# Kernel tuning notes

Hardware: AMD Instinct MI355X
Metric: run time of the kernel (lower is better)

Reference implementation:

```python
import jax, jax.numpy as jnp
import numpy as np

N_USERS = 50000
N_ITEMS = 10000
N_ENTITIES = 40000
N_NODES = N_USERS + N_ITEMS + N_ENTITIES  # 100000
EMB = 64
NNZ = 1600000  # avg degree 16
VIS_DIM = 2048
TXT_DIM = 300


def setup_inputs() -> dict:
    key = jax.random.key(0)
    ks = jax.random.split(key, 16)
    def xn(k, shape, scale=0.05):
        return jax.random.normal(k, shape, dtype=jnp.float32) * scale
    return {
        "adj_row": jax.random.randint(ks[0], (NNZ,), 0, N_NODES, dtype=jnp.int32),
        "adj_col": jax.random.randint(ks[1], (NNZ,), 0, N_NODES, dtype=jnp.int32),
        "adj_val": jax.random.uniform(ks[2], (NNZ,), dtype=jnp.float32) / 16.0,  # ~normalized adj
        "embedding": xn(ks[3], (N_NODES, EMB), 0.1),
        "visual_features": jax.random.normal(ks[4], (N_ITEMS, VIS_DIM), dtype=jnp.float32),
        "text_features": jax.random.normal(ks[5], (N_ITEMS, TXT_DIM), dtype=jnp.float32),
        "Wv1": xn(ks[6], (512, VIS_DIM)), "bv1": jnp.zeros((512,), jnp.float32),
        "Wv2": xn(ks[7], (EMB, 512)),    "bv2": jnp.zeros((EMB,), jnp.float32),
        "Wt1": xn(ks[8], (256, TXT_DIM)), "bt1": jnp.zeros((256,), jnp.float32),
        "Wt2": xn(ks[9], (EMB, 256)),    "bt2": jnp.zeros((EMB,), jnp.float32),
        "Wd": xn(ks[10], (EMB, EMB)),    "bd": jnp.zeros((EMB,), jnp.float32),
        "Wc0": xn(ks[11], (EMB, 2 * EMB)), "bc0": jnp.zeros((EMB,), jnp.float32),
        "Wc1": xn(ks[12], (EMB, 2 * EMB)), "bc1": jnp.zeros((EMB,), jnp.float32),
    }


def _lin(x, W, b):
    return x @ W.T + b


def reference(adj_row, adj_col, adj_val, embedding, visual_features, text_features,
              Wv1, bv1, Wv2, bv2, Wt1, bt1, Wt2, bt2, Wd, bd, Wc0, bc0, Wc1, bc1):
    # multimodal item encoding (eval mode: dropout = identity)
    vis = _lin(jax.nn.relu(_lin(visual_features, Wv1, bv1)), Wv2, bv2)
    vis = _lin(vis, Wd, bd)
    txt = _lin(jax.nn.relu(_lin(text_features, Wt1, bt1)), Wt2, bt2)
    txt = _lin(txt, Wd, bd)
    fused_item = (vis + txt) * 0.5  # [n_items, emb]

    ego = embedding.at[N_USERS:N_USERS + N_ITEMS].set(fused_item)

    all_embs = [ego]
    cur = ego
    for Wc, bc in ((Wc0, bc0), (Wc1, bc1)):
        # SpMM: neighbor[i] = sum_j A[i,j] * cur[j]
        msgs = adj_val[:, None] * cur[adj_col]            # [nnz, emb]
        nb = jax.ops.segment_sum(msgs, adj_row, num_segments=N_NODES)
        cur = _lin(jnp.concatenate([cur, nb], axis=-1), Wc, bc)  # W_concat
        cur = jax.nn.leaky_relu(cur, 0.01)                # F.leaky_relu default slope
        all_embs.append(cur)

    return jnp.concatenate(all_embs, axis=-1)  # [n_nodes, emb*(n_layers+1)]
```

## Files before the change

kernel.cpp:

```cpp
#include <hip/hip_runtime.h>
#include <hip/hip_bf16.h>
#include <cstddef>

#define N_USERS 50000
#define N_ITEMS 10000
#define N_NODES 100000
#define EMB 64
#define NNZ_E 1600000
#define VIS_DIM 2048
#define TXT_DIM 300

typedef short bf16x8 __attribute__((ext_vector_type(8)));
typedef float f32x4  __attribute__((ext_vector_type(4)));

__device__ inline unsigned short f2bf(float x) {
    __hip_bfloat16 h = __float2bfloat16(x);
    return __builtin_bit_cast(unsigned short, h);
}
__device__ inline float bf2f(unsigned short u) {
    unsigned int t = ((unsigned int)u) << 16;
    float f;
    __builtin_memcpy(&f, &t, 4);
    return f;
}

template<int MI, int NI>
__global__ __launch_bounds__(256) void gemm_dg(
    const float* __restrict__ A, const float* __restrict__ W,
    const float* __restrict__ bias, float* __restrict__ C,
    int M, int N, int K, int k_per, long long c_plane,
    int act, int add_bias)
{
    const int t   = threadIdx.x;
    const int w   = t >> 6;
    const int l   = t & 63;
    const int l16 = l & 15;
    const int lq  = l >> 4;

    const int n0 = blockIdx.x * (NI * 16);
    const int m0 = (blockIdx.y * 4 + w) * (MI * 16);
    if (m0 >= M) return;
    const int kz = blockIdx.z;
    const int kb = kz * k_per;
    int krem = K - kb; if (krem > k_per) krem = k_per;
    const int kiters = (krem + 31) / 32;
    float* Cz = C + (long long)kz * c_plane;

    const float* ap[MI];
    #pragma unroll
    for (int mi = 0; mi < MI; mi++) {
        int r = m0 + mi * 16 + l16; if (r >= M) r = M - 1;
        ap[mi] = A + (size_t)r * K;
    }
    const float* wpt[NI];
    #pragma unroll
    for (int ni = 0; ni < NI; ni++) {
        int r = n0 + ni * 16 + l16; if (r >= N) r = N - 1;
        wpt[ni] = W + (size_t)r * K;
    }

    f32x4 acc[MI][NI] = {};

    for (int kt = 0; kt < kiters; kt++) {
        const int k0 = kb + kt * 32 + lq * 8;

        bf16x8 ahi[MI], alo[MI];
        #pragma unroll
        for (int mi = 0; mi < MI; mi++) {
            float v[8];
            if (k0 + 7 < K) {
                float4 q0 = *(const float4*)(ap[mi] + k0);
                float4 q1 = *(const float4*)(ap[mi] + k0 + 4);
                v[0]=q0.x; v[1]=q0.y; v[2]=q0.z; v[3]=q0.w;
                v[4]=q1.x; v[5]=q1.y; v[6]=q1.z; v[7]=q1.w;
            } else {
                #pragma unroll
                for (int i = 0; i < 8; i++)
                    v[i] = (k0 + i < K) ? ap[mi][k0 + i] : 0.f;
            }
            #pragma unroll
            for (int i = 0; i < 8; i++) {
                unsigned short h = f2bf(v[i]);
                ahi[mi][i] = (short)h;
                alo[mi][i] = (short)f2bf(v[i] - bf2f(h));
            }
        }

        bf16x8 whi[NI], wlo[NI];
        #pragma unroll
        for (int ni = 0; ni < NI; ni++) {
            float v[8];
            if (k0 + 7 < K) {
                float4 q0 = *(const float4*)(wpt[ni] + k0);
                float4 q1 = *(const float4*)(wpt[ni] + k0 + 4);
                v[0]=q0.x; v[1]=q0.y; v[2]=q0.z; v[3]=q0.w;
                v[4]=q1.x; v[5]=q1.y; v[6]=q1.z; v[7]=q1.w;
            } else {
                #pragma unroll
                for (int i = 0; i < 8; i++)
                    v[i] = (k0 + i < K) ? wpt[ni][k0 + i] : 0.f;
            }
            #pragma unroll
            for (int i = 0; i < 8; i++) {
                unsigned short h = f2bf(v[i]);
                whi[ni][i] = (short)h;
                wlo[ni][i] = (short)f2bf(v[i] - bf2f(h));
            }
        }

        #pragma unroll
        for (int ni = 0; ni < NI; ni++) {
            #pragma unroll
            for (int mi = 0; mi < MI; mi++) {
                acc[mi][ni] = __builtin_amdgcn_mfma_f32_16x16x32_bf16(
                    ahi[mi], whi[ni], acc[mi][ni], 0, 0, 0);
                acc[mi][ni] = __builtin_amdgcn_mfma_f32_16x16x32_bf16(
                    ahi[mi], wlo[ni], acc[mi][ni], 0, 0, 0);
                acc[mi][ni] = __builtin_amdgcn_mfma_f32_16x16x32_bf16(
                    alo[mi], whi[ni], acc[mi][ni], 0, 0, 0);
            }
        }
    }

    #pragma unroll
    for (int ni = 0; ni < NI; ni++) {
        int col = n0 + ni * 16 + l16;
        if (col >= N) continue;
        float b = (add_bias && kz == 0) ? bias[col] : 0.f;
        #pragma unroll
        for (int mi = 0; mi < MI; mi++) {
            #pragma unroll
            for (int r = 0; r < 4; r++) {
                int row = m0 + mi * 16 + lq * 4 + r;
                if (row >= M) continue;
                float vv = acc[mi][ni][r] + b;
                if (act) vv = fmaxf(vv, 0.f);
                Cz[(size_t)row * N + col] = vv;
            }
        }
    }
}

#define GLDW 40

__global__ __launch_bounds__(256, 2) void concat_mfma(
    const float* __restrict__ cur, const float* __restrict__ nbuf,
    const float* __restrict__ Wc, const float* __restrict__ bias,
    float* __restrict__ out_cur, float* __restrict__ out_full, int col_off)
{
    __shared__ unsigned short Ah[128][GLDW], Al[128][GLDW];
    __shared__ unsigned short Bh[64][GLDW],  Bl[64][GLDW];

    const int t   = threadIdx.x;
    const int w   = t >> 6;
    const int l   = t & 63;
    const int l16 = l & 15;
    const int lq  = l >> 4;
    const int m0  = blockIdx.x * 128;
    const int mh  = w * 32;

    const int r  = t >> 2;
    const int kc = t & 3;

    f32x4 acc[2][4] = {};

    float pa[2][8], pw[8];

    auto load_tile = [&](int kt) {
        const float* src = (kt < 2) ? cur : nbuf;
        const int kcol = (kt & 1) * 32 + kc * 8;
        #pragma unroll
        for (int p = 0; p < 2; p++) {
            int rg = m0 + r + p * 64;
            if (rg >= N_NODES) rg = N_NODES - 1;
            const float* g = src + (size_t)rg * 64 + kcol;
            float4 q0 = *(const float4*)g, q1 = *(const float4*)(g + 4);
            pa[p][0]=q0.x; pa[p][1]=q0.y; pa[p][2]=q0.z; pa[p][3]=q0.w;
            pa[p][4]=q1.x; pa[p][5]=q1.y; pa[p][6]=q1.z; pa[p][7]=q1.w;
        }
        const float* gw = Wc + (size_t)r * 128 + kt * 32 + kc * 8;
        float4 q0 = *(const float4*)gw, q1 = *(const float4*)(gw + 4);
        pw[0]=q0.x; pw[1]=q0.y; pw[2]=q0.z; pw[3]=q0.w;
        pw[4]=q1.x; pw[5]=q1.y; pw[6]=q1.z; pw[7]=q1.w;
    };

    load_tile(0);

    for (int kt = 0; kt < 4; kt++) {
        #pragma unroll
        for (int p = 0; p < 2; p++) {
            bf16x8 hi, lo;
            #pragma unroll
            for (int i = 0; i < 8; i++) {
                unsigned short h = f2bf(pa[p][i]);
                hi[i] = (short)h;
                lo[i] = (short)f2bf(pa[p][i] - bf2f(h));
            }
            *(bf16x8*)&Ah[r + p * 64][kc * 8] = hi;
            *(bf16x8*)&Al[r + p * 64][kc * 8] = lo;
        }
        {
            bf16x8 hi, lo;
            #pragma unroll
            for (int i = 0; i < 8; i++) {
                unsigned short h = f2bf(pw[i]);
                hi[i] = (short)h;
                lo[i] = (short)f2bf(pw[i] - bf2f(h));
            }
            *(bf16x8*)&Bh[r][kc * 8] = hi;
            *(bf16x8*)&Bl[r][kc * 8] = lo;
        }
        __syncthreads();

        if (kt < 3) load_tile(kt + 1);

        {
            bf16x8 ah[2], al[2];
            #pragma unroll
            for (int mi = 0; mi < 2; mi++) {
                ah[mi] = *(const bf16x8*)&Ah[mh + mi * 16 + l16][lq * 8];
                al[mi] = *(const bf16x8*)&Al[mh + mi * 16 + l16][lq * 8];
            }
            #pragma unroll
            for (int ni = 0; ni < 4; ni++) {
                bf16x8 bh = *(const bf16x8*)&Bh[ni * 16 + l16][lq * 8];
                bf16x8 bl = *(const bf16x8*)&Bl[ni * 16 + l16][lq * 8];
                #pragma unroll
                for (int mi = 0; mi < 2; mi++) {
                    acc[mi][ni] = __builtin_amdgcn_mfma_f32_16x16x32_bf16(
                        ah[mi], bh, acc[mi][ni], 0, 0, 0);
                    acc[mi][ni] = __builtin_amdgcn_mfma_f32_16x16x32_bf16(
                        ah[mi], bl, acc[mi][ni], 0, 0, 0);
                    acc[mi][ni] = __builtin_amdgcn_mfma_f32_16x16x32_bf16(
                        al[mi], bh, acc[mi][ni], 0, 0, 0);
                }
            }
        }
        __syncthreads();
    }

    #pragma unroll
    for (int ni = 0; ni < 4; ni++) {
        int col = ni * 16 + l16;
        float bcol = bias[col];
        #pragma unroll
        for (int mi = 0; mi < 2; mi++) {
            #pragma unroll
            for (int rr = 0; rr < 4; rr++) {
                int row = m0 + mh + mi * 16 + lq * 4 + rr;
                if (row >= N_NODES) continue;
                float v = acc[mi][ni][rr] + bcol;
                v = (v > 0.f) ? v : 0.01f * v;
                if (out_cur) out_cur[(size_t)row * 64 + col] = v;
                out_full[(size_t)row * 192 + col_off + col] = v;
            }
        }
    }
}

__global__ void transp64(const float* __restrict__ W, float* __restrict__ wT, int K)
{
    int i = blockIdx.x * 256 + threadIdx.x;
    if (i >= 64 * K) return;
    int d = i / K, k = i - d * K;
    wT[k * 64 + d] = W[i];
}

__global__ __launch_bounds__(256) void linear64(
    const float* __restrict__ in, const float* __restrict__ in2,
    const float* __restrict__ wT, const float* __restrict__ bias,
    float* __restrict__ out, int M, int K, float in_scale, int add,
    int fuse_relu)
{
    int t  = threadIdx.x;
    int d  = t & 63;
    int w  = t >> 6;
    int m0 = blockIdx.x * 16 + w * 4;
    if (m0 >= M) return;
    int mlast = M - 1;
    int m1 = (m0 + 1 < M) ? m0 + 1 : mlast;
    int m2 = (m0 + 2 < M) ? m0 + 2 : mlast;
    int m3 = (m0 + 3 < M) ? m0 + 3 : mlast;

    const float* x0 = in + (size_t)m0 * K;
    const float* x1 = in + (size_t)m1 * K;
    const float* x2 = in + (size_t)m2 * K;
    const float* x3 = in + (size_t)m3 * K;
    const float* y0 = fuse_relu ? in2 + (size_t)m0 * K : x0;
    const float* y1 = fuse_relu ? in2 + (size_t)m1 * K : x1;
    const float* y2 = fuse_relu ? in2 + (size_t)m2 * K : x2;
    const float* y3 = fuse_relu ? in2 + (size_t)m3 * K : x3;

    float a0 = 0.f, a1 = 0.f, a2 = 0.f, a3 = 0.f;

    for (int k = 0; k < K; k += 8) {
        const float* wp = wT + (size_t)k * 64 + d;
        float w0 = wp[0],   w1 = wp[64],  w2 = wp[128], w3 = wp[192];
        float w4 = wp[256], w5 = wp[320], w6 = wp[384], w7 = wp[448];
        float4 p0 = *(const float4*)(x0 + k), q0 = *(const float4*)(x0 + k + 4);
        float4 p1 = *(const float4*)(x1 + k), q1 = *(const float4*)(x1 + k + 4);
        float4 p2 = *(const float4*)(x2 + k), q2 = *(const float4*)(x2 + k + 4);
        float4 p3 = *(const float4*)(x3 + k), q3 = *(const float4*)(x3 + k + 4);
        if (fuse_relu) {
            float4 r0 = *(const float4*)(y0 + k), s0 = *(const float4*)(y0 + k + 4);
            float4 r1 = *(const float4*)(y1 + k), s1 = *(const float4*)(y1 + k + 4);
            float4 r2 = *(const float4*)(y2 + k), s2 = *(const float4*)(y2 + k + 4);
            float4 r3 = *(const float4*)(y3 + k), s3 = *(const float4*)(y3 + k + 4);
            p0.x=fmaxf(p0.x+r0.x,0.f); p0.y=fmaxf(p0.y+r0.y,0.f);
            p0.z=fmaxf(p0.z+r0.z,0.f); p0.w=fmaxf(p0.w+r0.w,0.f);
            q0.x=fmaxf(q0.x+s0.x,0.f); q0.y=fmaxf(q0.y+s0.y,0.f);
            q0.z=fmaxf(q0.z+s0.z,0.f); q0.w=fmaxf(q0.w+s0.w,0.f);
            p1.x=fmaxf(p1.x+r1.x,0.f); p1.y=fmaxf(p1.y+r1.y,0.f);
            p1.z=fmaxf(p1.z+r1.z,0.f); p1.w=fmaxf(p1.w+r1.w,0.f);
            q1.x=fmaxf(q1.x+s1.x,0.f); q1.y=fmaxf(q1.y+s1.y,0.f);
            q1.z=fmaxf(q1.z+s1.z,0.f); q1.w=fmaxf(q1.w+s1.w,0.f);
            p2.x=fmaxf(p2.x+r2.x,0.f); p2.y=fmaxf(p2.y+r2.y,0.f);
            p2.z=fmaxf(p2.z+r2.z,0.f); p2.w=fmaxf(p2.w+r2.w,0.f);
            q2.x=fmaxf(q2.x+s2.x,0.f); q2.y=fmaxf(q2.y+s2.y,0.f);
            q2.z=fmaxf(q2.z+s2.z,0.f); q2.w=fmaxf(q2.w+s2.w,0.f);
            p3.x=fmaxf(p3.x+r3.x,0.f); p3.y=fmaxf(p3.y+r3.y,0.f);
            p3.z=fmaxf(p3.z+r3.z,0.f); p3.w=fmaxf(p3.w+r3.w,0.f);
            q3.x=fmaxf(q3.x+s3.x,0.f); q3.y=fmaxf(q3.y+s3.y,0.f);
            q3.z=fmaxf(q3.z+s3.z,0.f); q3.w=fmaxf(q3.w+s3.w,0.f);
        }
        a0 += p0.x*w0 + p0.y*w1 + p0.z*w2 + p0.w*w3
            + q0.x*w4 + q0.y*w5 + q0.z*w6 + q0.w*w7;
        a1 += p1.x*w0 + p1.y*w1 + p1.z*w2 + p1.w*w3
            + q1.x*w4 + q1.y*w5 + q1.z*w6 + q1.w*w7;
        a2 += p2.x*w0 + p2.y*w1 + p2.z*w2 + p2.w*w3
            + q2.x*w4 + q2.y*w5 + q2.z*w6 + q2.w*w7;
        a3 += p3.x*w0 + p3.y*w1 + p3.z*w2 + p3.w*w3
            + q3.x*w4 + q3.y*w5 + q3.z*w6 + q3.w*w7;
    }

    float b = bias[d];
    float r0 = a0 * in_scale + b;
    float r1 = a1 * in_scale + b;
    float r2 = a2 * in_scale + b;
    float r3 = a3 * in_scale + b;
    if (add) {
        out[(size_t)m0 * 64 + d] += r0;
        if (m0 + 1 < M) out[(size_t)m1 * 64 + d] += r1;
        if (m0 + 2 < M) out[(size_t)m2 * 64 + d] += r2;
        if (m0 + 3 < M) out[(size_t)m3 * 64 + d] += r3;
    } else {
        out[(size_t)m0 * 64 + d] = r0;
        if (m0 + 1 < M) out[(size_t)m1 * 64 + d] = r1;
        if (m0 + 2 < M) out[(size_t)m2 * 64 + d] = r2;
        if (m0 + 3 < M) out[(size_t)m3 * 64 + d] = r3;
    }
}

__global__ void ego_fill(const float* __restrict__ emb, float* __restrict__ cur0,
                         float* __restrict__ out_full)
{
    int tid = blockIdx.x * 256 + threadIdx.x;
    if (tid >= N_NODES * EMB) return;
    int m = tid >> 6, d = tid & 63;
    float v;
    if (m < N_USERS || m >= N_USERS + N_ITEMS) {
        v = emb[tid];
        cur0[tid] = v;
    } else {
        v = cur0[tid];
    }
    out_full[(size_t)m * 192 + d] = v;
}

__global__ __launch_bounds__(256) void hist_rows(
    const int* __restrict__ row, int* __restrict__ cnt, int nnz)
{
    int e = blockIdx.x * 256 + threadIdx.x;
    if (e >= nnz) return;
    atomicAdd(&cnt[row[e]], 1);
}

__global__ __launch_bounds__(256) void scan1(int* __restrict__ cnt,
                                             int* __restrict__ bsum, int n)
{
    __shared__ int part[256];
    int t = threadIdx.x;
    int base = blockIdx.x * 1024 + t * 4;
    int v0 = 0, v1 = 0, v2 = 0, v3 = 0;
    if (base + 0 < n) v0 = cnt[base + 0];
    if (base + 1 < n) v1 = cnt[base + 1];
    if (base + 2 < n) v2 = cnt[base + 2];
    if (base + 3 < n) v3 = cnt[base + 3];
    int s = v0 + v1 + v2 + v3;
    part[t] = s;
    __syncthreads();
    for (int off = 1; off < 256; off <<= 1) {
        int x = (t >= off) ? part[t - off] : 0;
        __syncthreads();
        part[t] += x;
        __syncthreads();
    }
    int excl = part[t] - s;
    if (t == 255) bsum[blockIdx.x] = part[t];
    if (base + 0 < n) cnt[base + 0] = excl;
    if (base + 1 < n) cnt[base + 1] = excl + v0;
    if (base + 2 < n) cnt[base + 2] = excl + v0 + v1;
    if (base + 3 < n) cnt[base + 3] = excl + v0 + v1 + v2;
}

__global__ void scan2(int* __restrict__ bsum, int nb)
{
    if (threadIdx.x == 0 && blockIdx.x == 0) {
        int acc = 0;
        for (int i = 0; i < nb; i++) { int v = bsum[i]; bsum[i] = acc; acc += v; }
    }
}

__global__ __launch_bounds__(256) void scan3(
    const int* __restrict__ excl, const int* __restrict__ bsum,
    int* __restrict__ row_ptr, int* __restrict__ row_cur, int n, int nnz)
{
    int i = blockIdx.x * 256 + threadIdx.x;
    if (i > n) return;
    if (i == n) { row_ptr[n] = nnz; return; }
    int v = excl[i] + bsum[i >> 10];
    row_ptr[i] = v;
    row_cur[i] = v;
}

__global__ __launch_bounds__(256) void scatter_csr(
    const int* __restrict__ row, const int* __restrict__ col,
    const float* __restrict__ val, int* __restrict__ row_cur,
    int* __restrict__ col_s, float* __restrict__ val_s, int nnz)
{
    int e = blockIdx.x * 256 + threadIdx.x;
    if (e >= nnz) return;
    int r = row[e];
    int p = atomicAdd(&row_cur[r], 1);
    col_s[p] = col[e];
    val_s[p] = val[e];
}

__global__ __launch_bounds__(256) void spmm_gather(
    const int* __restrict__ row_ptr, const int* __restrict__ col_s,
    const float* __restrict__ val_s, const float* __restrict__ cur,
    float* __restrict__ nb)
{
    int t  = threadIdx.x;
    int wv = t >> 6;
    int l  = t & 63;
    int eg = l >> 4;
    int dg = l & 15;
    int m = blockIdx.x * 4 + wv;
    if (m >= N_NODES) return;
    int beg = row_ptr[m], end = row_ptr[m + 1];
    float ax = 0.f, ay = 0.f, az = 0.f, aw = 0.f;
    for (int j = beg + eg; j < end; j += 4) {
        int   c = col_s[j];
        float v = val_s[j];
        float4 cv = *(const float4*)&cur[(size_t)c * 64 + dg * 4];
        ax += v * cv.x; ay += v * cv.y; az += v * cv.z; aw += v * cv.w;
    }
    ax += __shfl_xor(ax, 16, 64); ay += __shfl_xor(ay, 16, 64);
    az += __shfl_xor(az, 16, 64); aw += __shfl_xor(aw, 16, 64);
    ax += __shfl_xor(ax, 32, 64); ay += __shfl_xor(ay, 32, 64);
    az += __shfl_xor(az, 32, 64); aw += __shfl_xor(aw, 32, 64);
    if (eg == 0) {
        float4 r; r.x = ax; r.y = ay; r.z = az; r.w = aw;
        *(float4*)&nb[(size_t)m * 64 + dg * 4] = r;
    }
}

extern "C" void kernel_launch(void* const* d_in, const int* in_sizes, int n_in,
                              void* d_out, int out_size, void* d_ws, size_t ws_size,
                              hipStream_t stream)
{
    const int*   adj_row = (const int*)  d_in[0];
    const int*   adj_col = (const int*)  d_in[1];
    const float* adj_val = (const float*)d_in[2];
    const float* emb     = (const float*)d_in[3];
    const float* visf    = (const float*)d_in[4];
    const float* txtf    = (const float*)d_in[5];
    const float* Wv1 = (const float*)d_in[6];  const float* bv1 = (const float*)d_in[7];
    const float* Wv2 = (const float*)d_in[8];  const float* bv2 = (const float*)d_in[9];
    const float* Wt1 = (const float*)d_in[10]; const float* bt1 = (const float*)d_in[11];
    const float* Wt2 = (const float*)d_in[12]; const float* bt2 = (const float*)d_in[13];
    const float* Wd  = (const float*)d_in[14]; const float* bd  = (const float*)d_in[15];
    const float* Wc0 = (const float*)d_in[16]; const float* bc0 = (const float*)d_in[17];
    const float* Wc1 = (const float*)d_in[18]; const float* bc1 = (const float*)d_in[19];

    float* out = (float*)d_out;
    float* ws  = (float*)d_ws;

    float* H1v  = ws + 0;
    float* H1t  = ws + 5120000;
    float* nb   = ws + 0;
    float* s    = ws + 7680000;
    float* cur0 = ws + 8320000;
    float* cur1 = ws + 14720000;
    float* H1v2 = ws + 14720000;
    float* wv2T = ws + 21120000;
    float* wt2T = wv2T + 32768;
    float* wdT  = wt2T + 16384;
    int*   col_s   = (int*)  (ws + 21200000);
    float* val_s   =          ws + 22800000;
    int*   row_ptr = (int*)  (ws + 24400000);
    int*   row_cur = (int*)  (ws + 24510000);
    int*   cnt     = (int*)  (ws + 24620000);
    int*   bsum    = (int*)  (ws + 24730000);

    const int NBLK = (N_NODES + 1023) / 1024;

    transp64<<<(64 * 512 + 255) / 256, 256, 0, stream>>>(Wv2, wv2T, 512);
    transp64<<<(64 * 256 + 255) / 256, 256, 0, stream>>>(Wt2, wt2T, 256);
    transp64<<<(64 * 64  + 255) / 256, 256, 0, stream>>>(Wd,  wdT,  64);

    hipMemsetAsync(cnt, 0, N_NODES * sizeof(int), stream);
    hist_rows<<<(NNZ_E + 255) / 256, 256, 0, stream>>>(adj_row, cnt, NNZ_E);
    scan1<<<NBLK, 256, 0, stream>>>(cnt, bsum, N_NODES);
    scan2<<<1, 64, 0, stream>>>(bsum, NBLK);
    scan3<<<(N_NODES + 256) / 256, 256, 0, stream>>>(cnt, bsum, row_ptr, row_cur,
                                                     N_NODES, NNZ_E);
    scatter_csr<<<(NNZ_E + 255) / 256, 256, 0, stream>>>(adj_row, adj_col, adj_val,
                                                         row_cur, col_s, val_s, NNZ_E);

    {
        dim3 g(512 / 64, (157 + 3) / 4, 2);
        gemm_dg<4, 4><<<g, 256, 0, stream>>>(visf, Wv1, bv1, H1v,
                                             N_ITEMS, 512, VIS_DIM,
                                             1024, (long long)14720000,
                                             0, 1);
    }
    {
        dim3 g(256 / 32, (313 + 3) / 4, 1);
        gemm_dg<2, 2><<<g, 256, 0, stream>>>(txtf, Wt1, bt1, H1t,
                                             N_ITEMS, 256, TXT_DIM,
                                             512, 0, 1, 1);
    }

    linear64<<<(N_ITEMS + 15) / 16, 256, 0, stream>>>(H1v, H1v2, wv2T, bv2, s,
                                                      N_ITEMS, 512, 1.0f, 0, 1);
    linear64<<<(N_ITEMS + 15) / 16, 256, 0, stream>>>(H1t, nullptr, wt2T, bt2, s,
                                                      N_ITEMS, 256, 1.0f, 1, 0);
    linear64<<<(N_ITEMS + 15) / 16, 256, 0, stream>>>(s, nullptr, wdT, bd,
                                                      cur0 + (size_t)N_USERS * 64,
                                                      N_ITEMS, 64, 0.5f, 0, 0);

    ego_fill<<<(N_NODES * EMB + 255) / 256, 256, 0, stream>>>(emb, cur0, out);

    spmm_gather<<<(N_NODES + 3) / 4, 256, 0, stream>>>(row_ptr, col_s, val_s, cur0, nb);
    concat_mfma<<<(N_NODES + 127) / 128, 256, 0, stream>>>(cur0, nb, Wc0, bc0, cur1, out, 64);

    spmm_gather<<<(N_NODES + 3) / 4, 256, 0, stream>>>(row_ptr, col_s, val_s, cur1, nb);
    concat_mfma<<<(N_NODES + 127) / 128, 256, 0, stream>>>(cur1, nb, Wc1, bc1, nullptr, out, 128);
}
```

Measured before the change: 987.1 us.

## Stage split-bf16 GEMM tiles through LDS with register prefetch

Replaces the direct-from-global register GEMM for the visual and text first-layer projections with a 128x64 block tile staged in shared memory. The fp32 to hi/lo bf16 split is now done once per element per block rather than redundantly in each wave. The next k-tile is prefetched into registers while the MFMAs run. This is meant to cut global load traffic and duplicated conversion work in the largest GEMM (10000x512x2048), at the cost of two barriers per k-step and LDS usage that may limit occupancy.

```diff
diff --git a/kernel.cpp b/kernel.cpp
--- a/kernel.cpp
+++ b/kernel.cpp
@@ -24,124 +24,145 @@
     return f;
 }
 
-template<int MI, int NI>
-__global__ __launch_bounds__(256) void gemm_dg(
+#define GLDW 40
+
+__global__ __launch_bounds__(256, 2) void gemm_bf64(
     const float* __restrict__ A, const float* __restrict__ W,
     const float* __restrict__ bias, float* __restrict__ C,
     int M, int N, int K, int k_per, long long c_plane,
     int act, int add_bias)
 {
+    __shared__ unsigned short Ah[128][GLDW], Al[128][GLDW];
+    __shared__ unsigned short Bh[64][GLDW],  Bl[64][GLDW];
+
     const int t   = threadIdx.x;
     const int w   = t >> 6;
     const int l   = t & 63;
     const int l16 = l & 15;
     const int lq  = l >> 4;
-
-    const int n0 = blockIdx.x * (NI * 16);
-    const int m0 = (blockIdx.y * 4 + w) * (MI * 16);
-    if (m0 >= M) return;
-    const int kz = blockIdx.z;
-    const int kb = kz * k_per;
+    const int n0  = blockIdx.x * 64;
+    const int m0  = blockIdx.y * 128;
+    const int mh  = w * 32;
+
+    const int kz  = blockIdx.z;
+    const int kb  = kz * k_per;
     int krem = K - kb; if (krem > k_per) krem = k_per;
     const int kiters = (krem + 31) / 32;
+    const int kend = kb + krem;
     float* Cz = C + (long long)kz * c_plane;
 
-    const float* ap[MI];
-    #pragma unroll
-    for (int mi = 0; mi < MI; mi++) {
-        int r = m0 + mi * 16 + l16; if (r >= M) r = M - 1;
-        ap[mi] = A + (size_t)r * K;
-    }
-    const float* wpt[NI];
-    #pragma unroll
-    for (int ni = 0; ni < NI; ni++) {
-        int r = n0 + ni * 16 + l16; if (r >= N) r = N - 1;
-        wpt[ni] = W + (size_t)r * K;
-    }
-
-    f32x4 acc[MI][NI] = {};
-
-    for (int kt = 0; kt < kiters; kt++) {
-        const int k0 = kb + kt * 32 + lq * 8;
-
-        bf16x8 ahi[MI], alo[MI];
+    const int rA0 = t >> 2;
+    const int rA1 = (t + 256) >> 2;
+    const int kc  = t & 3;
+
+    f32x4 acc[2][4] = {};
+    float pa[2][8], pw[8];
+
+    auto load_tile = [&](int kt) {
+        const int k0 = kb + kt * 32 + kc * 8;
         #pragma unroll
-        for (int mi = 0; mi < MI; mi++) {
-            float v[8];
-            if (k0 + 7 < K) {
-                float4 q0 = *(const float4*)(ap[mi] + k0);
-                float4 q1 = *(const float4*)(ap[mi] + k0 + 4);
-                v[0]=q0.x; v[1]=q0.y; v[2]=q0.z; v[3]=q0.w;
-                v[4]=q1.x; v[5]=q1.y; v[6]=q1.z; v[7]=q1.w;
+        for (int p = 0; p < 2; p++) {
+            int rg = m0 + (p ? rA1 : rA0);
+            if (rg >= M) rg = M - 1;
+            const float* g = A + (size_t)rg * K + k0;
+            if (k0 + 7 < kend) {
+                float4 q0 = *(const float4*)g, q1 = *(const float4*)(g + 4);
+                pa[p][0]=q0.x; pa[p][1]=q0.y; pa[p][2]=q0.z; pa[p][3]=q0.w;
+                pa[p][4]=q1.x; pa[p][5]=q1.y; pa[p][6]=q1.z; pa[p][7]=q1.w;
             } else {
                 #pragma unroll
                 for (int i = 0; i < 8; i++)
-                    v[i] = (k0 + i < K) ? ap[mi][k0 + i] : 0.f;
-            }
+                    pa[p][i] = (k0 + i < kend) ? g[i] : 0.f;
+            }
+        }
+        int ng = n0 + rA0;
+        if (ng >= N) ng = N - 1;
+        const float* gw = W + (size_t)ng * K + k0;
+        if (k0 + 7 < kend) {
+            float4 q0 = *(const float4*)gw, q1 = *(const float4*)(gw + 4);
+            pw[0]=q0.x; pw[1]=q0.y; pw[2]=q0.z; pw[3]=q0.w;
+            pw[4]=q1.x; pw[5]=q1.y; pw[6]=q1.z; pw[7]=q1.w;
+        } else {
+            #pragma unroll
+            for (int i = 0; i < 8; i++)
+                pw[i] = (k0 + i < kend) ? gw[i] : 0.f;
+        }
+    };
+
+    load_tile(0);
+
+    for (int kt = 0; kt < kiters; kt++) {
+        #pragma unroll
+        for (int p = 0; p < 2; p++) {
+            int row = p ? rA1 : rA0;
+            bf16x8 hi, lo;
             #pragma unroll
             for (int i = 0; i < 8; i++) {
-                unsigned short h = f2bf(v[i]);
-                ahi[mi][i] = (short)h;
-                alo[mi][i] = (short)f2bf(v[i] - bf2f(h));
-            }
-        }
-
-        bf16x8 whi[NI], wlo[NI];
-        #pragma unroll
-        for (int ni = 0; ni < NI; ni++) {
-            float v[8];
-            if (k0 + 7 < K) {
-                float4 q0 = *(const float4*)(wpt[ni] + k0);
-                float4 q1 = *(const float4*)(wpt[ni] + k0 + 4);
-                v[0]=q0.x; v[1]=q0.y; v[2]=q0.z; v[3]=q0.w;
-                v[4]=q1.x; v[5]=q1.y; v[6]=q1.z; v[7]=q1.w;
-            } else {
+                unsigned short h = f2bf(pa[p][i]);
+                hi[i] = (short)h;
+                lo[i] = (short)f2bf(pa[p][i] - bf2f(h));
+            }
+            *(bf16x8*)&Ah[row][kc * 8] = hi;
+            *(bf16x8*)&Al[row][kc * 8] = lo;
+        }
+        {
+            bf16x8 hi, lo;
+            #pragma unroll
+            for (int i = 0; i < 8; i++) {
+                unsigned short h = f2bf(pw[i]);
+                hi[i] = (short)h;
+                lo[i] = (short)f2bf(pw[i] - bf2f(h));
+            }
+            *(bf16x8*)&Bh[rA0][kc * 8] = hi;
+            *(bf16x8*)&Bl[rA0][kc * 8] = lo;
+        }
+        __syncthreads();
+
+        if (kt + 1 < kiters) load_tile(kt + 1);
+
+        {
+            bf16x8 ah[2], al[2];
+            #pragma unroll
+            for (int mi = 0; mi < 2; mi++) {
+                ah[mi] = *(const bf16x8*)&Ah[mh + mi * 16 + l16][lq * 8];
+                al[mi] = *(const bf16x8*)&Al[mh + mi * 16 + l16][lq * 8];
+            }
+            #pragma unroll
+            for (int ni = 0; ni < 4; ni++) {
+                bf16x8 bh = *(const bf16x8*)&Bh[ni * 16 + l16][lq * 8];
+                bf16x8 bl = *(const bf16x8*)&Bl[ni * 16 + l16][lq * 8];
                 #pragma unroll
-                for (int i = 0; i < 8; i++)
-                    v[i] = (k0 + i < K) ? wpt[ni][k0 + i] : 0.f;
-            }
-            #pragma unroll
-            for (int i = 0; i < 8; i++) {
-                unsigned short h = f2bf(v[i]);
-                whi[ni][i] = (short)h;
-                wlo[ni][i] = (short)f2bf(v[i] - bf2f(h));
-            }
-        }
-
-        #pragma unroll
-        for (int ni = 0; ni < NI; ni++) {
-            #pragma unroll
-            for (int mi = 0; mi < MI; mi++) {
-                acc[mi][ni] = __builtin_amdgcn_mfma_f32_16x16x32_bf16(
-                    ahi[mi], whi[ni], acc[mi][ni], 0, 0, 0);
-                acc[mi][ni] = __builtin_amdgcn_mfma_f32_16x16x32_bf16(
-                    ahi[mi], wlo[ni], acc[mi][ni], 0, 0, 0);
-                acc[mi][ni] = __builtin_amdgcn_mfma_f32_16x16x32_bf16(
-                    alo[mi], whi[ni], acc[mi][ni], 0, 0, 0);
-            }
-        }
+                for (int mi = 0; mi < 2; mi++) {
+                    acc[mi][ni] = __builtin_amdgcn_mfma_f32_16x16x32_bf16(
+                        ah[mi], bh, acc[mi][ni], 0, 0, 0);
+                    acc[mi][ni] = __builtin_amdgcn_mfma_f32_16x16x32_bf16(
+                        ah[mi], bl, acc[mi][ni], 0, 0, 0);
+                    acc[mi][ni] = __builtin_amdgcn_mfma_f32_16x16x32_bf16(
+                        al[mi], bh, acc[mi][ni], 0, 0, 0);
+                }
+            }
+        }
+        __syncthreads();
     }
 
     #pragma unroll
-    for (int ni = 0; ni < NI; ni++) {
+    for (int ni = 0; ni < 4; ni++) {
         int col = n0 + ni * 16 + l16;
         if (col >= N) continue;
         float b = (add_bias && kz == 0) ? bias[col] : 0.f;
         #pragma unroll
-        for (int mi = 0; mi < MI; mi++) {
+        for (int mi = 0; mi < 2; mi++) {
             #pragma unroll
             for (int r = 0; r < 4; r++) {
-                int row = m0 + mi * 16 + lq * 4 + r;
+                int row = m0 + mh + mi * 16 + lq * 4 + r;
                 if (row >= M) continue;
-                float vv = acc[mi][ni][r] + b;
-                if (act) vv = fmaxf(vv, 0.f);
-                Cz[(size_t)row * N + col] = vv;
-            }
-        }
-    }
-}
-
-#define GLDW 40
+                float v = acc[mi][ni][r] + b;
+                if (act) v = fmaxf(v, 0.f);
+                Cz[(size_t)row * N + col] = v;
+            }
+        }
+    }
+}
 
 __global__ __launch_bounds__(256, 2) void concat_mfma(
     const float* __restrict__ cur, const float* __restrict__ nbuf,
@@ -520,17 +541,16 @@
                                                          row_cur, col_s, val_s, NNZ_E);
 
     {
-        dim3 g(512 / 64, (157 + 3) / 4, 2);
-        gemm_dg<4, 4><<<g, 256, 0, stream>>>(visf, Wv1, bv1, H1v,
-                                             N_ITEMS, 512, VIS_DIM,
-                                             1024, (long long)14720000,
-                                             0, 1);
+        dim3 g(512 / 64, (N_ITEMS + 127) / 128, 2);
+        gemm_bf64<<<g, 256, 0, stream>>>(visf, Wv1, bv1, H1v,
+                                         N_ITEMS, 512, VIS_DIM,
+                                         1024, (long long)14720000, 0, 1);
     }
     {
-        dim3 g(256 / 32, (313 + 3) / 4, 1);
-        gemm_dg<2, 2><<<g, 256, 0, stream>>>(txtf, Wt1, bt1, H1t,
-                                             N_ITEMS, 256, TXT_DIM,
-                                             512, 0, 1, 1);
+        dim3 g(256 / 64, (N_ITEMS + 127) / 128, 1);
+        gemm_bf64<<<g, 256, 0, stream>>>(txtf, Wt1, bt1, H1t,
+                                         N_ITEMS, 256, TXT_DIM,
+                                         512, 0, 1, 1);
     }
 
     linear64<<<(N_ITEMS + 15) / 16, 256, 0, stream>>>(H1v, H1v2, wv2T, bv2, s,
```

After: 831.3 us. 15.8% less time.
